# Optimization experiments

Hardware: AMD Instinct MI355X
Metric: run time of the kernel (lower is better)

The kernel has to match this reference:

```python
import jax, jax.numpy as jnp
import numpy as np

# Acoustic FDTD constants (seistorch-style geometry)
NSHOTS, NT = 4, 512
NZ, NX = 256, 256
NRECS = 128
DT = 1e-3   # s
DH = 10.0   # m grid spacing


def setup_inputs() -> dict:
    key = jax.random.key(0)
    k1, k2, k3, k4, k5, k6 = jax.random.split(key, 6)
    x = jax.random.normal(k1, (NSHOTS, NT), dtype=jnp.float32)  # source wavelets
    # velocity model in [1500, 4000] m/s (CFL: dt*vmax/dh = 0.4 < stability limit)
    vp = 1500.0 + 2500.0 * jax.random.uniform(k2, (NZ, NX), dtype=jnp.float32)
    src_z = jax.random.randint(k3, (NSHOTS,), 0, NZ)
    src_x = jax.random.randint(k4, (NSHOTS,), 0, NX)
    rec_z = jax.random.randint(k5, (NSHOTS, NRECS), 0, NZ)
    rec_x = jax.random.randint(k6, (NSHOTS, NRECS), 0, NX)
    return {"x": x, "vp": vp, "src_z": src_z, "src_x": src_x,
            "rec_z": rec_z, "rec_x": rec_x}


def _laplacian(p):
    # 5-point stencil, zero Dirichlet boundary. p: (B, NZ, NX)
    pp = jnp.pad(p, ((0, 0), (1, 1), (1, 1)))
    return (pp[:, 2:, 1:-1] + pp[:, :-2, 1:-1]
            + pp[:, 1:-1, 2:] + pp[:, 1:-1, :-2]
            - 4.0 * p) / (DH * DH)


def reference(x, vp, src_z, src_x, rec_z, rec_x):
    shots = jnp.arange(NSHOTS)
    c2dt2 = (vp * DT) ** 2  # (NZ, NX), broadcast over shots

    def step(carry, wav_t):
        p_prev, p = carry
        # 2nd-order acoustic update (the PDE "cell")
        p_next = 2.0 * p - p_prev + c2dt2 * _laplacian(p)
        # source scatter-inject (super_source)
        p_next = p_next.at[shots, src_z, src_x].add(wav_t * DT * DT)
        # receiver gather (super_probes): (NSHOTS, NRECS)
        rec = p_next[shots[:, None], rec_z, rec_x]
        return (p, p_next), rec

    p0 = jnp.zeros((NSHOTS, NZ, NX), dtype=x.dtype)
    _, recs = jax.lax.scan(step, (p0, p0), x.T)  # recs: (NT, NSHOTS, NRECS)
    # (shots, time, receivers, n_receiver_types=1)
    return jnp.transpose(recs, (1, 0, 2))[..., None]
```

## Files before the change

### kernel.cpp

```cpp
#include <hip/hip_runtime.h>

#define NSHOTS 4
#define NT     512
#define NZ     256
#define NX     256
#define NRECS  128

static constexpr float DTf    = 0.001f;
static constexpr float INVDH2 = 1.0f / (10.0f * 10.0f);

#define KSTEPS 16
#define TILE   32
#define RPT    8
#define NPAIRS 4
#define NWAVES 8
#define BLOCK  512
#define NWG    (NSHOTS * 64)
#define NPHASE (NT / KSTEPS)

typedef float v2f __attribute__((ext_vector_type(2)));
typedef unsigned long long ull;

__device__ __forceinline__ float nbr_left(float v) {
  return __int_as_float(__builtin_amdgcn_update_dpp(
      0, __float_as_int(v), 0x138 , 0xf, 0xf, true));
}
__device__ __forceinline__ float nbr_right(float v) {
  return __int_as_float(__builtin_amdgcn_update_dpp(
      0, __float_as_int(v), 0x130 , 0xf, 0xf, true));
}

__device__ __forceinline__ ull pload(const ull* p) {
  return __hip_atomic_load(p, __ATOMIC_RELAXED, __HIP_MEMORY_SCOPE_AGENT);
}
__device__ __forceinline__ void pstore(ull* p, ull v) {
  __hip_atomic_store(p, v, __ATOMIC_RELAXED, __HIP_MEMORY_SCOPE_AGENT);
}

__device__ __forceinline__ ull pack_w(float cur, float prev, unsigned tg) {
  const unsigned hi = (__float_as_uint(prev) & ~3u) | tg;
  return ((ull)hi << 32) | (ull)__float_as_uint(cur);
}
__device__ __forceinline__ float w_cur(ull w) {
  return __uint_as_float((unsigned)w);
}
__device__ __forceinline__ float w_prev(ull w) {
  return __uint_as_float(((unsigned)(w >> 32)) & ~3u);
}
__device__ __forceinline__ unsigned tag_of(int q) {
  return ((unsigned)(q >> 1) % 3u) + 1u;
}

__global__ __launch_bounds__(BLOCK, 4) void wave_pk(
    ull* __restrict__ gA, ull* __restrict__ gB,
    const float* __restrict__ vp, const float* __restrict__ xwav,
    const int* __restrict__ src_z, const int* __restrict__ src_x,
    const int* __restrict__ rec_z, const int* __restrict__ rec_x,
    float* __restrict__ out)
{
  const int bid  = blockIdx.x;
  const int s    = bid >> 6;
  const int tz   = (bid >> 3) & 7;
  const int tx   = bid & 7;
  const int tid  = threadIdx.x;
  const int w    = tid >> 6;
  const int lane = tid & 63;

  const int gz0 = tz * TILE - KSTEPS;
  const int gx0 = tx * TILE - KSTEPS;
  const int gx  = gx0 + lane;
  const int zb  = w * RPT;

  __shared__ float haloTop[2][NWAVES][64];
  __shared__ float haloBot[2][NWAVES][64];
  __shared__ float recTile[2][TILE][TILE + 1];
  __shared__ int   cntS;
  __shared__ int   lzA[NRECS], lxA[NRECS];
  __shared__ unsigned pkA[NRECS];

  if (tid == 0) cntS = 0;
  __syncthreads();
  if (tid < NRECS) {
    const int lz = rec_z[s * NRECS + tid] - tz * TILE;
    const int lx = rec_x[s * NRECS + tid] - tx * TILE;
    lzA[tid] = lz; lxA[tid] = lx;
    if ((unsigned)lz < (unsigned)TILE && (unsigned)lx < (unsigned)TILE) {
      const int k = atomicAdd(&cntS, 1);
      pkA[k] = (unsigned)tid | ((unsigned)lz << 8) | ((unsigned)lx << 16);
    }
  }
  __syncthreads();
  const int nRec = cntS;
  int myR = 0, myLz = 0, myLx = 0;
  if (tid < nRec) {
    const unsigned p = pkA[tid];
    myR = p & 255; myLz = (p >> 8) & 31; myLx = (p >> 16) & 31;
  }
  const bool wbRow = (w >= 2 && w < 6) && (lane >= KSTEPS && lane < KSTEPS + TILE);
  const int  ilz   = (w - 2) * RPT;
  const int  ilx   = lane - KSTEPS;
  unsigned recMask = 0;
  if (wbRow) {
    for (int r = 0; r < NRECS; ++r)
      if (lxA[r] == ilx && (unsigned)(lzA[r] - ilz) < (unsigned)RPT)
        recMask |= 1u << (lzA[r] - ilz);
  }

  const int slz = src_z[s] - gz0;
  const int slx = src_x[s] - gx0;
  const bool srcMine = (slx == lane) && ((unsigned)(slz - zb) < (unsigned)RPT);
  const int  srcI = slz - zb;
  v2f srcM2[NPAIRS];
  #pragma unroll
  for (int p = 0; p < NPAIRS; ++p) {
    srcM2[p].x = (srcMine && srcI == 2 * p)     ? 1.0f : 0.0f;
    srcM2[p].y = (srcMine && srcI == 2 * p + 1) ? 1.0f : 0.0f;
  }

  const bool xok = (unsigned)gx < (unsigned)NX;
  int   offRow[RPT];
  bool  okRow[RPT];
  v2f a2[NPAIRS], b2[NPAIRS], c22[NPAIRS], d22[NPAIRS];
  unsigned okMask = 0;
  #pragma unroll
  for (int p = 0; p < NPAIRS; ++p) {
    #pragma unroll
    for (int h = 0; h < 2; ++h) {
      const int i  = 2 * p + h;
      const int gz = gz0 + zb + i;
      const bool ok = xok && ((unsigned)gz < (unsigned)NZ);
      okRow[i]  = ok;
      if (ok) okMask |= 1u << i;
      offRow[i] = ok ? ((s * NZ + gz) * NX + gx) : 0;
      float v = ok ? vp[gz * NX + gx] : 0.0f;
      v *= DTf;
      const float c2 = v * v * INVDH2;
      if (h == 0) { c22[p].x = c2; d22[p].x = 2.0f - 4.0f * c2; }
      else        { c22[p].y = c2; d22[p].y = 2.0f - 4.0f * c2; }
    }
    a2[p] = (v2f)(0.0f); b2[p] = (v2f)(0.0f);
  }

  #pragma unroll 1
  for (int ph = 0; ph < NPHASE; ++ph) {
    const int t0 = ph * KSTEPS;

    float amp[KSTEPS];
    {
      const float4* xw4 = (const float4*)(xwav + s * NT + t0);
      #pragma unroll
      for (int q = 0; q < KSTEPS / 4; ++q) {
        const float4 v = xw4[q];
        amp[4 * q + 0] = (v.x * DTf) * DTf;
        amp[4 * q + 1] = (v.y * DTf) * DTf;
        amp[4 * q + 2] = (v.z * DTf) * DTf;
        amp[4 * q + 3] = (v.w * DTf) * DTf;
      }
    }

    if (ph > 0 && !wbRow) {
      const ull* gR = (ph & 1) ? gA : gB;
      const unsigned tg = tag_of(ph - 1);
      ull vw[RPT];
      unsigned need = okMask;
      while (need) {
        ull t[RPT];
        #pragma unroll
        for (int i = 0; i < RPT; ++i)
          if (need & (1u << i)) t[i] = pload(gR + offRow[i]);
        #pragma unroll
        for (int i = 0; i < RPT; ++i)
          if ((need & (1u << i)) && (((unsigned)(t[i] >> 32)) & 3u) == tg) {
            vw[i] = t[i];
            need &= ~(1u << i);
          }
        if (need) __builtin_amdgcn_s_sleep(1);
      }
      #pragma unroll
      for (int i = 0; i < RPT; ++i) {
        const float cv = okRow[i] ? w_cur(vw[i])  : 0.0f;
        const float pv = okRow[i] ? w_prev(vw[i]) : 0.0f;
        if (i & 1) { a2[i >> 1].y = cv; b2[i >> 1].y = pv; }
        else       { a2[i >> 1].x = cv; b2[i >> 1].x = pv; }
      }
    }

    float recv[KSTEPS];

    auto do_step = [&](v2f (&cur)[NPAIRS], v2f (&nxt)[NPAIRS], int tau) {
      const int pb = tau & 1;
      haloTop[pb][w][lane] = cur[0].x;
      haloBot[pb][w][lane] = cur[NPAIRS - 1].y;
      __syncthreads();
      if (tau > 0 && tid < nRec) recv[tau - 1] = recTile[1 - pb][myLz][myLx];
      const float up0 = (w > 0)          ? haloBot[pb][w - 1][lane] : 0.0f;
      const float dn7 = (w < NWAVES - 1) ? haloTop[pb][w + 1][lane] : 0.0f;
      const v2f av = { amp[tau], amp[tau] };
      #pragma unroll
      for (int p = 0; p < NPAIRS; ++p) {
        const float cx = cur[p].x, cy = cur[p].y;
        const float upx = (p == 0)          ? up0 : cur[p - 1].y;
        const float dny = (p == NPAIRS - 1) ? dn7 : cur[p + 1].x;
        v2f ud, lr;
        ud.x = upx + cy;
        ud.y = cx + dny;
        lr.x = nbr_left(cx) + nbr_right(cx);
        lr.y = nbr_left(cy) + nbr_right(cy);
        const v2f sum = ud + lr;
        v2f t = __builtin_elementwise_fma(c22[p], sum, -nxt[p]);
        t = __builtin_elementwise_fma(d22[p], cur[p], t);
        t = __builtin_elementwise_fma(srcM2[p], av, t);
        nxt[p] = t;
      }
      if (recMask) {
        #pragma unroll
        for (int i = 0; i < RPT; ++i)
          if (recMask & (1u << i))
            recTile[pb][ilz + i][ilx] = (i & 1) ? nxt[i >> 1].y : nxt[i >> 1].x;
      }
    };

    #pragma unroll
    for (int h = 0; h < KSTEPS / 2; ++h) {
      do_step(a2, b2, 2 * h);
      do_step(b2, a2, 2 * h + 1);
    }

    if (ph != NPHASE - 1) {
      ull* gW = (ph & 1) ? gB : gA;
      const unsigned tgw = tag_of(ph);
      if (wbRow) {
        #pragma unroll
        for (int p = 0; p < NPAIRS; ++p) {
          pstore(gW + offRow[2 * p],     pack_w(a2[p].x, b2[p].x, tgw));
          pstore(gW + offRow[2 * p + 1], pack_w(a2[p].y, b2[p].y, tgw));
        }
      }
    }
    __syncthreads();

    if (tid < nRec) {
      recv[KSTEPS - 1] = recTile[1][myLz][myLx];
      #pragma unroll
      for (int t = 0; t < KSTEPS; ++t)
        out[(s * NT + (t0 + t)) * NRECS + myR] = recv[t];
    }
  }
}

extern "C" void kernel_launch(void* const* d_in, const int* in_sizes, int n_in,
                              void* d_out, int out_size, void* d_ws, size_t ws_size,
                              hipStream_t stream) {
  const float* x     = (const float*)d_in[0];
  const float* vp    = (const float*)d_in[1];
  const int*   src_z = (const int*)d_in[2];
  const int*   src_x = (const int*)d_in[3];
  const int*   rec_z = (const int*)d_in[4];
  const int*   rec_x = (const int*)d_in[5];
  float* out = (float*)d_out;

  const size_t F = (size_t)NSHOTS * NZ * NX;
  ull* gA = (ull*)d_ws;
  ull* gB = gA + F;

  hipMemsetAsync(gA, 0, 2 * F * sizeof(ull), stream);

  wave_pk<<<dim3(NWG), dim3(BLOCK), 0, stream>>>(
      gA, gB, vp, x, src_z, src_x, rec_z, rec_x, out);
}
```

Before: 303.8 us.

## Widen per-wave slabs with two-row ghosts to sync once per two steps

Each wave now holds its 8-row slab plus two ghost rows on each side (12 rows in 6 pairs). Halos are exchanged through shared memory only every two time steps, which halves the number of block barriers. Receiver values are written straight to global memory from the owning lane each step, replacing the shared recTile staging and per-phase flush. The source amplitude is loaded and injected only in the wave that owns the source. In exchange there is redundant stencil work on the ghost rows, higher register pressure, and launch bounds lowered from 4 to 2 blocks per CU, which may reduce occupancy.

```diff
diff --git a/kernel.cpp b/kernel.cpp
--- a/kernel.cpp
+++ b/kernel.cpp
@@ -11,8 +11,8 @@
 
 #define KSTEPS 16
 #define TILE   32
-#define RPT    8
-#define NPAIRS 4
+#define SLAB   8
+#define WPAIR  6
 #define NWAVES 8
 #define BLOCK  512
 #define NWG    (NSHOTS * 64)
@@ -51,7 +51,7 @@
   return ((unsigned)(q >> 1) % 3u) + 1u;
 }
 
-__global__ __launch_bounds__(BLOCK, 4) void wave_pk(
+__global__ __launch_bounds__(BLOCK, 2) void wave_pk(
     ull* __restrict__ gA, ull* __restrict__ gB,
     const float* __restrict__ vp, const float* __restrict__ xwav,
     const int* __restrict__ src_z, const int* __restrict__ src_x,
@@ -69,69 +69,31 @@
   const int gz0 = tz * TILE - KSTEPS;
   const int gx0 = tx * TILE - KSTEPS;
   const int gx  = gx0 + lane;
-  const int zb  = w * RPT;
-
-  __shared__ float haloTop[2][NWAVES][64];
-  __shared__ float haloBot[2][NWAVES][64];
-  __shared__ float recTile[2][TILE][TILE + 1];
-  __shared__ int   cntS;
-  __shared__ int   lzA[NRECS], lxA[NRECS];
-  __shared__ unsigned pkA[NRECS];
-
-  if (tid == 0) cntS = 0;
-  __syncthreads();
-  if (tid < NRECS) {
-    const int lz = rec_z[s * NRECS + tid] - tz * TILE;
-    const int lx = rec_x[s * NRECS + tid] - tx * TILE;
-    lzA[tid] = lz; lxA[tid] = lx;
-    if ((unsigned)lz < (unsigned)TILE && (unsigned)lx < (unsigned)TILE) {
-      const int k = atomicAdd(&cntS, 1);
-      pkA[k] = (unsigned)tid | ((unsigned)lz << 8) | ((unsigned)lx << 16);
-    }
-  }
-  __syncthreads();
-  const int nRec = cntS;
-  int myR = 0, myLz = 0, myLx = 0;
-  if (tid < nRec) {
-    const unsigned p = pkA[tid];
-    myR = p & 255; myLz = (p >> 8) & 31; myLx = (p >> 16) & 31;
-  }
-  const bool wbRow = (w >= 2 && w < 6) && (lane >= KSTEPS && lane < KSTEPS + TILE);
-  const int  ilz   = (w - 2) * RPT;
-  const int  ilx   = lane - KSTEPS;
-  unsigned recMask = 0;
-  if (wbRow) {
-    for (int r = 0; r < NRECS; ++r)
-      if (lxA[r] == ilx && (unsigned)(lzA[r] - ilz) < (unsigned)RPT)
-        recMask |= 1u << (lzA[r] - ilz);
-  }
-
-  const int slz = src_z[s] - gz0;
-  const int slx = src_x[s] - gx0;
-  const bool srcMine = (slx == lane) && ((unsigned)(slz - zb) < (unsigned)RPT);
-  const int  srcI = slz - zb;
-  v2f srcM2[NPAIRS];
-  #pragma unroll
-  for (int p = 0; p < NPAIRS; ++p) {
-    srcM2[p].x = (srcMine && srcI == 2 * p)     ? 1.0f : 0.0f;
-    srcM2[p].y = (srcMine && srcI == 2 * p + 1) ? 1.0f : 0.0f;
-  }
-
+  const int zb  = w * SLAB;
   const bool xok = (unsigned)gx < (unsigned)NX;
-  int   offRow[RPT];
-  bool  okRow[RPT];
-  v2f a2[NPAIRS], b2[NPAIRS], c22[NPAIRS], d22[NPAIRS];
+
+  __shared__ float xchC[2][NWAVES][4][64];
+  __shared__ float xchP[NWAVES][2][64];
+  __shared__ int   lzS[NRECS], lxS[NRECS];
+
+  int offRow[SLAB];
   unsigned okMask = 0;
   #pragma unroll
-  for (int p = 0; p < NPAIRS; ++p) {
+  for (int k = 0; k < SLAB; ++k) {
+    const int gz = gz0 + zb + k;
+    const bool ok = xok && (unsigned)gz < (unsigned)NZ;
+    offRow[k] = ok ? ((s * NZ + gz) * NX + gx) : 0;
+    if (ok) okMask |= 1u << k;
+  }
+
+  v2f c22[WPAIR], d22[WPAIR], a2[WPAIR], b2[WPAIR];
+  #pragma unroll
+  for (int p = 0; p < WPAIR; ++p) {
     #pragma unroll
     for (int h = 0; h < 2; ++h) {
-      const int i  = 2 * p + h;
-      const int gz = gz0 + zb + i;
-      const bool ok = xok && ((unsigned)gz < (unsigned)NZ);
-      okRow[i]  = ok;
-      if (ok) okMask |= 1u << i;
-      offRow[i] = ok ? ((s * NZ + gz) * NX + gx) : 0;
+      const int e  = zb - 2 + 2 * p + h;
+      const int gz = gz0 + e;
+      const bool ok = ((unsigned)e < 64u) && xok && ((unsigned)gz < (unsigned)NZ);
       float v = ok ? vp[gz * NX + gx] : 0.0f;
       v *= DTf;
       const float c2 = v * v * INVDH2;
@@ -141,12 +103,126 @@
     a2[p] = (v2f)(0.0f); b2[p] = (v2f)(0.0f);
   }
 
+  const bool wbT = (w >= 2 && w < 6) && (lane >= KSTEPS && lane < KSTEPS + TILE);
+
+  if (tid < NRECS) {
+    lzS[tid] = rec_z[s * NRECS + tid] - tz * TILE;
+    lxS[tid] = rec_x[s * NRECS + tid] - tx * TILE;
+  }
+  __syncthreads();
+  unsigned e0 = 0, e1 = 0, rB0 = 0, rB1 = 0, rB2 = 0, rB3 = 0;
+  if (wbT) {
+    int cnt = 0;
+    #pragma unroll 1
+    for (int r = 0; r < NRECS; ++r) {
+      const int er = lzS[r], ex = lxS[r];
+      if ((unsigned)er < (unsigned)TILE && (unsigned)ex < (unsigned)TILE) {
+        const int extz = er + KSTEPS;
+        if ((extz >> 3) == w && ex + KSTEPS == lane) {
+          const int wr = extz - zb + 2;
+          const unsigned e = 0x8000u | ((unsigned)wr << 8) | (unsigned)r;
+          if (cnt == 0) e0 = e;
+          else if (cnt == 1) e1 = e;
+          else {
+            if (r < 32)      rB0 |= 1u << r;
+            else if (r < 64) rB1 |= 1u << (r - 32);
+            else if (r < 96) rB2 |= 1u << (r - 64);
+            else             rB3 |= 1u << (r - 96);
+          }
+          ++cnt;
+        }
+      }
+    }
+  }
+  const bool hasOvf = (rB0 | rB1 | rB2 | rB3) != 0;
+
+  const int slz = src_z[s] - gz0;
+  const int slx = src_x[s] - gx0;
+  const int srcRow = slz - (zb - 2);
+  const bool hasSrc = ((unsigned)slz < 64u) && ((unsigned)slx < 64u) &&
+                      ((unsigned)srcRow < 12u);
+  const bool srcLane = (slx == lane);
+
+  float amp[KSTEPS];
+
+  auto selSlab = [](const v2f (&n)[WPAIR], int wr) -> float {
+    const int q = (wr >> 1) - 1;
+    const v2f pA = (q & 1) ? n[2] : n[1];
+    const v2f pB = (q & 1) ? n[4] : n[3];
+    const v2f pp = (q & 2) ? pB : pA;
+    return (wr & 1) ? pp.y : pp.x;
+  };
+
+  auto do_step = [&](v2f (&cur)[WPAIR], v2f (&nxt)[WPAIR], int tau, int t0) {
+    #pragma unroll
+    for (int p = 0; p < WPAIR; ++p) {
+      const float cx = cur[p].x, cy = cur[p].y;
+      const float upx = (p == 0)         ? 0.0f : cur[p - 1].y;
+      const float dny = (p == WPAIR - 1) ? 0.0f : cur[p + 1].x;
+      v2f ud, lr;
+      ud.x = upx + cy;
+      ud.y = cx + dny;
+      lr.x = nbr_left(cx) + nbr_right(cx);
+      lr.y = nbr_left(cy) + nbr_right(cy);
+      const v2f sum = ud + lr;
+      v2f t = __builtin_elementwise_fma(c22[p], sum, -nxt[p]);
+      t = __builtin_elementwise_fma(d22[p], cur[p], t);
+      nxt[p] = t;
+    }
+    if (hasSrc) {
+      const float av = amp[tau];
+      #pragma unroll
+      for (int p = 0; p < WPAIR; ++p) {
+        if (srcLane && srcRow == 2 * p)     nxt[p].x += av;
+        if (srcLane && srcRow == 2 * p + 1) nxt[p].y += av;
+      }
+    }
+    const int t = t0 + tau;
+    if (e0 & 0x8000u)
+      out[(s * NT + t) * NRECS + (e0 & 127u)] = selSlab(nxt, (e0 >> 8) & 15);
+    if (e1 & 0x8000u)
+      out[(s * NT + t) * NRECS + (e1 & 127u)] = selSlab(nxt, (e1 >> 8) & 15);
+    if (hasOvf) {
+      #pragma unroll
+      for (int wd = 0; wd < 4; ++wd) {
+        unsigned m = (wd == 0) ? rB0 : (wd == 1) ? rB1 : (wd == 2) ? rB2 : rB3;
+        while (m) {
+          const int b = __builtin_ctz(m); m &= m - 1;
+          const int r = wd * 32 + b;
+          const int wr = lzS[r] + KSTEPS - zb + 2;
+          out[(s * NT + t) * NRECS + r] = selSlab(nxt, wr);
+        }
+      }
+    }
+  };
+
+  auto exchange = [&](int buf, bool withPrev) {
+    xchC[buf][w][0][lane] = a2[1].x;
+    xchC[buf][w][1][lane] = a2[1].y;
+    xchC[buf][w][2][lane] = a2[4].x;
+    xchC[buf][w][3][lane] = a2[4].y;
+    if (withPrev) {
+      xchP[w][0][lane] = b2[1].x;
+      xchP[w][1][lane] = b2[4].y;
+    }
+    __syncthreads();
+    if (w > 0) {
+      a2[0].x = xchC[buf][w - 1][2][lane];
+      a2[0].y = xchC[buf][w - 1][3][lane];
+      if (withPrev) b2[0].y = xchP[w - 1][1][lane];
+    }
+    if (w < NWAVES - 1) {
+      a2[5].x = xchC[buf][w + 1][0][lane];
+      a2[5].y = xchC[buf][w + 1][1][lane];
+      if (withPrev) b2[5].x = xchP[w + 1][0][lane];
+    }
+  };
+
   #pragma unroll 1
   for (int ph = 0; ph < NPHASE; ++ph) {
     const int t0 = ph * KSTEPS;
 
-    float amp[KSTEPS];
-    {
+    if (hasSrc) {
       const float4* xw4 = (const float4*)(xwav + s * NT + t0);
       #pragma unroll
       for (int q = 0; q < KSTEPS / 4; ++q) {
@@ -158,18 +234,18 @@
       }
     }
 
-    if (ph > 0 && !wbRow) {
+    if (ph > 0 && !wbT) {
       const ull* gR = (ph & 1) ? gA : gB;
       const unsigned tg = tag_of(ph - 1);
-      ull vw[RPT];
+      ull vw[SLAB];
       unsigned need = okMask;
       while (need) {
-        ull t[RPT];
+        ull t[SLAB];
         #pragma unroll
-        for (int i = 0; i < RPT; ++i)
+        for (int i = 0; i < SLAB; ++i)
           if (need & (1u << i)) t[i] = pload(gR + offRow[i]);
         #pragma unroll
-        for (int i = 0; i < RPT; ++i)
+        for (int i = 0; i < SLAB; ++i)
           if ((need & (1u << i)) && (((unsigned)(t[i] >> 32)) & 3u) == tg) {
             vw[i] = t[i];
             need &= ~(1u << i);
@@ -177,73 +253,33 @@
         if (need) __builtin_amdgcn_s_sleep(1);
       }
       #pragma unroll
-      for (int i = 0; i < RPT; ++i) {
-        const float cv = okRow[i] ? w_cur(vw[i])  : 0.0f;
-        const float pv = okRow[i] ? w_prev(vw[i]) : 0.0f;
-        if (i & 1) { a2[i >> 1].y = cv; b2[i >> 1].y = pv; }
-        else       { a2[i >> 1].x = cv; b2[i >> 1].x = pv; }
-      }
-    }
-
-    float recv[KSTEPS];
-
-    auto do_step = [&](v2f (&cur)[NPAIRS], v2f (&nxt)[NPAIRS], int tau) {
-      const int pb = tau & 1;
-      haloTop[pb][w][lane] = cur[0].x;
-      haloBot[pb][w][lane] = cur[NPAIRS - 1].y;
-      __syncthreads();
-      if (tau > 0 && tid < nRec) recv[tau - 1] = recTile[1 - pb][myLz][myLx];
-      const float up0 = (w > 0)          ? haloBot[pb][w - 1][lane] : 0.0f;
-      const float dn7 = (w < NWAVES - 1) ? haloTop[pb][w + 1][lane] : 0.0f;
-      const v2f av = { amp[tau], amp[tau] };
-      #pragma unroll
-      for (int p = 0; p < NPAIRS; ++p) {
-        const float cx = cur[p].x, cy = cur[p].y;
-        const float upx = (p == 0)          ? up0 : cur[p - 1].y;
-        const float dny = (p == NPAIRS - 1) ? dn7 : cur[p + 1].x;
-        v2f ud, lr;
-        ud.x = upx + cy;
-        ud.y = cx + dny;
-        lr.x = nbr_left(cx) + nbr_right(cx);
-        lr.y = nbr_left(cy) + nbr_right(cy);
-        const v2f sum = ud + lr;
-        v2f t = __builtin_elementwise_fma(c22[p], sum, -nxt[p]);
-        t = __builtin_elementwise_fma(d22[p], cur[p], t);
-        t = __builtin_elementwise_fma(srcM2[p], av, t);
-        nxt[p] = t;
-      }
-      if (recMask) {
-        #pragma unroll
-        for (int i = 0; i < RPT; ++i)
-          if (recMask & (1u << i))
-            recTile[pb][ilz + i][ilx] = (i & 1) ? nxt[i >> 1].y : nxt[i >> 1].x;
-      }
-    };
+      for (int k = 0; k < SLAB; ++k) {
+        const bool ok = (okMask >> k) & 1;
+        const float cv = ok ? w_cur(vw[k])  : 0.0f;
+        const float pv = ok ? w_prev(vw[k]) : 0.0f;
+        const int p = 1 + (k >> 1);
+        if (k & 1) { a2[p].y = cv; b2[p].y = pv; }
+        else       { a2[p].x = cv; b2[p].x = pv; }
+      }
+    }
 
     #pragma unroll
-    for (int h = 0; h < KSTEPS / 2; ++h) {
-      do_step(a2, b2, 2 * h);
-      do_step(b2, a2, 2 * h + 1);
-    }
-
-    if (ph != NPHASE - 1) {
+    for (int blk = 0; blk < KSTEPS / 2; ++blk) {
+      exchange(blk & 1, blk == 0);
+      do_step(a2, b2, 2 * blk,     t0);
+      do_step(b2, a2, 2 * blk + 1, t0);
+    }
+
+    if (ph != NPHASE - 1 && wbT) {
       ull* gW = (ph & 1) ? gB : gA;
       const unsigned tgw = tag_of(ph);
-      if (wbRow) {
-        #pragma unroll
-        for (int p = 0; p < NPAIRS; ++p) {
-          pstore(gW + offRow[2 * p],     pack_w(a2[p].x, b2[p].x, tgw));
-          pstore(gW + offRow[2 * p + 1], pack_w(a2[p].y, b2[p].y, tgw));
-        }
-      }
-    }
-    __syncthreads();
-
-    if (tid < nRec) {
-      recv[KSTEPS - 1] = recTile[1][myLz][myLx];
-      #pragma unroll
-      for (int t = 0; t < KSTEPS; ++t)
-        out[(s * NT + (t0 + t)) * NRECS + myR] = recv[t];
+      #pragma unroll
+      for (int k = 0; k < SLAB; ++k) {
+        const int p = 1 + (k >> 1);
+        const float cv = (k & 1) ? a2[p].y : a2[p].x;
+        const float pv = (k & 1) ? b2[p].y : b2[p].x;
+        pstore(gW + offRow[k], pack_w(cv, pv, tgw));
+      }
     }
   }
 }
```

Result: slower. 358.9 us (+18.2%).

## Replace per-step block barriers with neighbor-wave LDS flag synchronization

Applied to the files above, without the earlier changes.

Each time step previously ended in a workgroup-wide __syncthreads. Now each wave waits only on its two vertical neighbor waves through per-wave LDS flags with acquire/release semantics. Receiver samples are written straight to global memory by the owning lane instead of staging through a shared tile. Source injection and wavelet loads are restricted to the wave that contains the source. Launch bounds drop from 4 to 2 blocks per SM, and the spin-waiting can stall or cost issue slots if waves drift apart.

```diff
diff --git a/kernel.cpp b/kernel.cpp
--- a/kernel.cpp
+++ b/kernel.cpp
@@ -17,6 +17,7 @@
 #define BLOCK  512
 #define NWG    (NSHOTS * 64)
 #define NPHASE (NT / KSTEPS)
+#define FSTR   32
 
 typedef float v2f __attribute__((ext_vector_type(2)));
 typedef unsigned long long ull;
@@ -51,7 +52,14 @@
   return ((unsigned)(q >> 1) % 3u) + 1u;
 }
 
-__global__ __launch_bounds__(BLOCK, 4) void wave_pk(
+__device__ __forceinline__ int lflag(const int* p) {
+  return __hip_atomic_load(p, __ATOMIC_ACQUIRE, __HIP_MEMORY_SCOPE_WORKGROUP);
+}
+__device__ __forceinline__ void sflag(int* p, int v) {
+  __hip_atomic_store(p, v, __ATOMIC_RELEASE, __HIP_MEMORY_SCOPE_WORKGROUP);
+}
+
+__global__ __launch_bounds__(BLOCK, 2) void wave_pk(
     ull* __restrict__ gA, ull* __restrict__ gB,
     const float* __restrict__ vp, const float* __restrict__ xwav,
     const int* __restrict__ src_z, const int* __restrict__ src_x,
@@ -71,55 +79,25 @@
   const int gx  = gx0 + lane;
   const int zb  = w * RPT;
 
-  __shared__ float haloTop[2][NWAVES][64];
-  __shared__ float haloBot[2][NWAVES][64];
-  __shared__ float recTile[2][TILE][TILE + 1];
-  __shared__ int   cntS;
-  __shared__ int   lzA[NRECS], lxA[NRECS];
-  __shared__ unsigned pkA[NRECS];
-
-  if (tid == 0) cntS = 0;
-  __syncthreads();
+  __shared__ float hT[2][NWAVES][64];
+  __shared__ float hB[2][NWAVES][64];
+  __shared__ int   wfl[NWAVES * FSTR];
+  __shared__ int   lzS[NRECS], lxS[NRECS];
+
   if (tid < NRECS) {
-    const int lz = rec_z[s * NRECS + tid] - tz * TILE;
-    const int lx = rec_x[s * NRECS + tid] - tx * TILE;
-    lzA[tid] = lz; lxA[tid] = lx;
-    if ((unsigned)lz < (unsigned)TILE && (unsigned)lx < (unsigned)TILE) {
-      const int k = atomicAdd(&cntS, 1);
-      pkA[k] = (unsigned)tid | ((unsigned)lz << 8) | ((unsigned)lx << 16);
-    }
-  }
-  __syncthreads();
-  const int nRec = cntS;
-  int myR = 0, myLz = 0, myLx = 0;
-  if (tid < nRec) {
-    const unsigned p = pkA[tid];
-    myR = p & 255; myLz = (p >> 8) & 31; myLx = (p >> 16) & 31;
-  }
-  const bool wbRow = (w >= 2 && w < 6) && (lane >= KSTEPS && lane < KSTEPS + TILE);
-  const int  ilz   = (w - 2) * RPT;
-  const int  ilx   = lane - KSTEPS;
-  unsigned recMask = 0;
-  if (wbRow) {
-    for (int r = 0; r < NRECS; ++r)
-      if (lxA[r] == ilx && (unsigned)(lzA[r] - ilz) < (unsigned)RPT)
-        recMask |= 1u << (lzA[r] - ilz);
-  }
-
-  const int slz = src_z[s] - gz0;
-  const int slx = src_x[s] - gx0;
-  const bool srcMine = (slx == lane) && ((unsigned)(slz - zb) < (unsigned)RPT);
-  const int  srcI = slz - zb;
-  v2f srcM2[NPAIRS];
-  #pragma unroll
-  for (int p = 0; p < NPAIRS; ++p) {
-    srcM2[p].x = (srcMine && srcI == 2 * p)     ? 1.0f : 0.0f;
-    srcM2[p].y = (srcMine && srcI == 2 * p + 1) ? 1.0f : 0.0f;
-  }
+    lzS[tid] = rec_z[s * NRECS + tid] - tz * TILE;
+    lxS[tid] = rec_x[s * NRECS + tid] - tx * TILE;
+  }
+  hT[0][w][lane] = 0.0f; hB[0][w][lane] = 0.0f;
+  hT[1][w][lane] = 0.0f; hB[1][w][lane] = 0.0f;
+  if (lane == 0)
+    __hip_atomic_store(&wfl[w * FSTR], 0, __ATOMIC_RELAXED,
+                       __HIP_MEMORY_SCOPE_WORKGROUP);
+
+  const bool wbT = (w >= 2 && w < 6) && (lane >= KSTEPS && lane < KSTEPS + TILE);
 
   const bool xok = (unsigned)gx < (unsigned)NX;
   int   offRow[RPT];
-  bool  okRow[RPT];
   v2f a2[NPAIRS], b2[NPAIRS], c22[NPAIRS], d22[NPAIRS];
   unsigned okMask = 0;
   #pragma unroll
@@ -129,7 +107,6 @@
       const int i  = 2 * p + h;
       const int gz = gz0 + zb + i;
       const bool ok = xok && ((unsigned)gz < (unsigned)NZ);
-      okRow[i]  = ok;
       if (ok) okMask |= 1u << i;
       offRow[i] = ok ? ((s * NZ + gz) * NX + gx) : 0;
       float v = ok ? vp[gz * NX + gx] : 0.0f;
@@ -141,12 +118,114 @@
     a2[p] = (v2f)(0.0f); b2[p] = (v2f)(0.0f);
   }
 
+  const int slz = src_z[s] - gz0;
+  const int slx = src_x[s] - gx0;
+  const bool hasSrcW = ((unsigned)slx < 64u) &&
+                       ((unsigned)(slz - zb) < (unsigned)RPT);
+  const bool srcMine = hasSrcW && (slx == lane);
+  const int  srcI = slz - zb;
+  v2f srcM2[NPAIRS];
+  #pragma unroll
+  for (int p = 0; p < NPAIRS; ++p) {
+    srcM2[p].x = (srcMine && srcI == 2 * p)     ? 1.0f : 0.0f;
+    srcM2[p].y = (srcMine && srcI == 2 * p + 1) ? 1.0f : 0.0f;
+  }
+
+  __syncthreads();
+
+  unsigned e0 = 0, e1 = 0, rB0 = 0, rB1 = 0, rB2 = 0, rB3 = 0;
+  if (wbT) {
+    int cnt = 0;
+    #pragma unroll 1
+    for (int r = 0; r < NRECS; ++r) {
+      const int er = lzS[r], ex = lxS[r];
+      if ((unsigned)er < (unsigned)TILE && (unsigned)ex < (unsigned)TILE) {
+        const int extz = er + KSTEPS;
+        if ((extz >> 3) == w && ex + KSTEPS == lane) {
+          const unsigned e = 0x8000u | ((unsigned)(extz & 7) << 8) | (unsigned)r;
+          if (cnt == 0) e0 = e;
+          else if (cnt == 1) e1 = e;
+          else {
+            if (r < 32)      rB0 |= 1u << r;
+            else if (r < 64) rB1 |= 1u << (r - 32);
+            else if (r < 96) rB2 |= 1u << (r - 64);
+            else             rB3 |= 1u << (r - 96);
+          }
+          ++cnt;
+        }
+      }
+    }
+  }
+  const bool hasOvf = (rB0 | rB1 | rB2 | rB3) != 0;
+
+  float amp[KSTEPS];
+
+  auto selRow = [](const v2f (&n)[NPAIRS], int row) -> float {
+    const v2f pA = (row & 2) ? n[1] : n[0];
+    const v2f pB = (row & 2) ? n[3] : n[2];
+    const v2f pp = (row & 4) ? pB : pA;
+    return (row & 1) ? pp.y : pp.x;
+  };
+
+  auto do_step = [&](v2f (&cur)[NPAIRS], v2f (&nxt)[NPAIRS], int tau, int t0) {
+    const int tg = t0 + tau + 1;
+    if (w > 0)
+      while (lflag(&wfl[(w - 1) * FSTR]) < tg - 1) {}
+    if (w < NWAVES - 1)
+      while (lflag(&wfl[(w + 1) * FSTR]) < tg - 1) {}
+    const int rs = (tg - 1) & 1;
+    const float up0 = (w > 0)          ? hB[rs][w - 1][lane] : 0.0f;
+    const float dn7 = (w < NWAVES - 1) ? hT[rs][w + 1][lane] : 0.0f;
+    #pragma unroll
+    for (int p = 0; p < NPAIRS; ++p) {
+      const float cx = cur[p].x, cy = cur[p].y;
+      const float upx = (p == 0)          ? up0 : cur[p - 1].y;
+      const float dny = (p == NPAIRS - 1) ? dn7 : cur[p + 1].x;
+      v2f ud, lr;
+      ud.x = upx + cy;
+      ud.y = cx + dny;
+      lr.x = nbr_left(cx) + nbr_right(cx);
+      lr.y = nbr_left(cy) + nbr_right(cy);
+      const v2f sum = ud + lr;
+      v2f t = __builtin_elementwise_fma(c22[p], sum, -nxt[p]);
+      t = __builtin_elementwise_fma(d22[p], cur[p], t);
+      nxt[p] = t;
+    }
+    if (hasSrcW) {
+      const v2f av = { amp[tau], amp[tau] };
+      #pragma unroll
+      for (int p = 0; p < NPAIRS; ++p)
+        nxt[p] = __builtin_elementwise_fma(srcM2[p], av, nxt[p]);
+    }
+    if (tau != KSTEPS - 1) {
+      const int ws2 = tg & 1;
+      hT[ws2][w][lane] = nxt[0].x;
+      hB[ws2][w][lane] = nxt[NPAIRS - 1].y;
+      if (lane == 0) sflag(&wfl[w * FSTR], tg);
+    }
+    const int t = t0 + tau;
+    if (e0 & 0x8000u)
+      out[(s * NT + t) * NRECS + (e0 & 127u)] = selRow(nxt, (e0 >> 8) & 7);
+    if (e1 & 0x8000u)
+      out[(s * NT + t) * NRECS + (e1 & 127u)] = selRow(nxt, (e1 >> 8) & 7);
+    if (hasOvf) {
+      #pragma unroll
+      for (int wd = 0; wd < 4; ++wd) {
+        unsigned m = (wd == 0) ? rB0 : (wd == 1) ? rB1 : (wd == 2) ? rB2 : rB3;
+        while (m) {
+          const int b = __builtin_ctz(m); m &= m - 1;
+          const int r = wd * 32 + b;
+          out[(s * NT + t) * NRECS + r] = selRow(nxt, (lzS[r] + KSTEPS) & 7);
+        }
+      }
+    }
+  };
+
   #pragma unroll 1
   for (int ph = 0; ph < NPHASE; ++ph) {
     const int t0 = ph * KSTEPS;
 
-    float amp[KSTEPS];
-    {
+    if (hasSrcW) {
       const float4* xw4 = (const float4*)(xwav + s * NT + t0);
       #pragma unroll
       for (int q = 0; q < KSTEPS / 4; ++q) {
@@ -158,92 +237,53 @@
       }
     }
 
-    if (ph > 0 && !wbRow) {
-      const ull* gR = (ph & 1) ? gA : gB;
-      const unsigned tg = tag_of(ph - 1);
-      ull vw[RPT];
-      unsigned need = okMask;
-      while (need) {
-        ull t[RPT];
+    if (ph > 0) {
+      if (!wbT) {
+        const ull* gR = (ph & 1) ? gA : gB;
+        const unsigned tg = tag_of(ph - 1);
+        ull vw[RPT];
+        unsigned need = okMask;
+        while (need) {
+          ull t[RPT];
+          #pragma unroll
+          for (int i = 0; i < RPT; ++i)
+            if (need & (1u << i)) t[i] = pload(gR + offRow[i]);
+          #pragma unroll
+          for (int i = 0; i < RPT; ++i)
+            if ((need & (1u << i)) && (((unsigned)(t[i] >> 32)) & 3u) == tg) {
+              vw[i] = t[i];
+              need &= ~(1u << i);
+            }
+          if (need) __builtin_amdgcn_s_sleep(1);
+        }
         #pragma unroll
-        for (int i = 0; i < RPT; ++i)
-          if (need & (1u << i)) t[i] = pload(gR + offRow[i]);
-        #pragma unroll
-        for (int i = 0; i < RPT; ++i)
-          if ((need & (1u << i)) && (((unsigned)(t[i] >> 32)) & 3u) == tg) {
-            vw[i] = t[i];
-            need &= ~(1u << i);
-          }
-        if (need) __builtin_amdgcn_s_sleep(1);
-      }
-      #pragma unroll
-      for (int i = 0; i < RPT; ++i) {
-        const float cv = okRow[i] ? w_cur(vw[i])  : 0.0f;
-        const float pv = okRow[i] ? w_prev(vw[i]) : 0.0f;
-        if (i & 1) { a2[i >> 1].y = cv; b2[i >> 1].y = pv; }
-        else       { a2[i >> 1].x = cv; b2[i >> 1].x = pv; }
-      }
-    }
-
-    float recv[KSTEPS];
-
-    auto do_step = [&](v2f (&cur)[NPAIRS], v2f (&nxt)[NPAIRS], int tau) {
-      const int pb = tau & 1;
-      haloTop[pb][w][lane] = cur[0].x;
-      haloBot[pb][w][lane] = cur[NPAIRS - 1].y;
-      __syncthreads();
-      if (tau > 0 && tid < nRec) recv[tau - 1] = recTile[1 - pb][myLz][myLx];
-      const float up0 = (w > 0)          ? haloBot[pb][w - 1][lane] : 0.0f;
-      const float dn7 = (w < NWAVES - 1) ? haloTop[pb][w + 1][lane] : 0.0f;
-      const v2f av = { amp[tau], amp[tau] };
+        for (int i = 0; i < RPT; ++i) {
+          const bool ok = (okMask >> i) & 1;
+          const float cv = ok ? w_cur(vw[i])  : 0.0f;
+          const float pv = ok ? w_prev(vw[i]) : 0.0f;
+          if (i & 1) { a2[i >> 1].y = cv; b2[i >> 1].y = pv; }
+          else       { a2[i >> 1].x = cv; b2[i >> 1].x = pv; }
+        }
+      }
+      hT[0][w][lane] = a2[0].x;
+      hB[0][w][lane] = a2[NPAIRS - 1].y;
+      if (lane == 0) sflag(&wfl[w * FSTR], t0);
+    }
+
+    #pragma unroll
+    for (int h = 0; h < KSTEPS / 2; ++h) {
+      do_step(a2, b2, 2 * h,     t0);
+      do_step(b2, a2, 2 * h + 1, t0);
+    }
+
+    if (ph != NPHASE - 1 && wbT) {
+      ull* gW = (ph & 1) ? gB : gA;
+      const unsigned tgw = tag_of(ph);
       #pragma unroll
       for (int p = 0; p < NPAIRS; ++p) {
-        const float cx = cur[p].x, cy = cur[p].y;
-        const float upx = (p == 0)          ? up0 : cur[p - 1].y;
-        const float dny = (p == NPAIRS - 1) ? dn7 : cur[p + 1].x;
-        v2f ud, lr;
-        ud.x = upx + cy;
-        ud.y = cx + dny;
-        lr.x = nbr_left(cx) + nbr_right(cx);
-        lr.y = nbr_left(cy) + nbr_right(cy);
-        const v2f sum = ud + lr;
-        v2f t = __builtin_elementwise_fma(c22[p], sum, -nxt[p]);
-        t = __builtin_elementwise_fma(d22[p], cur[p], t);
-        t = __builtin_elementwise_fma(srcM2[p], av, t);
-        nxt[p] = t;
-      }
-      if (recMask) {
-        #pragma unroll
-        for (int i = 0; i < RPT; ++i)
-          if (recMask & (1u << i))
-            recTile[pb][ilz + i][ilx] = (i & 1) ? nxt[i >> 1].y : nxt[i >> 1].x;
-      }
-    };
-
-    #pragma unroll
-    for (int h = 0; h < KSTEPS / 2; ++h) {
-      do_step(a2, b2, 2 * h);
-      do_step(b2, a2, 2 * h + 1);
-    }
-
-    if (ph != NPHASE - 1) {
-      ull* gW = (ph & 1) ? gB : gA;
-      const unsigned tgw = tag_of(ph);
-      if (wbRow) {
-        #pragma unroll
-        for (int p = 0; p < NPAIRS; ++p) {
-          pstore(gW + offRow[2 * p],     pack_w(a2[p].x, b2[p].x, tgw));
-          pstore(gW + offRow[2 * p + 1], pack_w(a2[p].y, b2[p].y, tgw));
-        }
-      }
-    }
-    __syncthreads();
-
-    if (tid < nRec) {
-      recv[KSTEPS - 1] = recTile[1][myLz][myLx];
-      #pragma unroll
-      for (int t = 0; t < KSTEPS; ++t)
-        out[(s * NT + (t0 + t)) * NRECS + myR] = recv[t];
+        pstore(gW + offRow[2 * p],     pack_w(a2[p].x, b2[p].x, tgw));
+        pstore(gW + offRow[2 * p + 1], pack_w(a2[p].y, b2[p].y, tgw));
+      }
     }
   }
 }
```

Measured after the change: 316.5 us. 4.2% more time.

## Interleave two shots per workgroup with flag-based wave sync and smaller tiles

Applied to the files above, without the earlier changes.

Each workgroup now handles two shots on 16x32 tiles with 8-step temporal blocking, and interleaves the two shots' time steps offset by half a phase. The goal is to hide global halo exchange latency behind the other shot's compute. Per-step __syncthreads is replaced with per-wave LDS flags for neighbour-only sync. Receiver values are written directly from registers instead of through a shared tile, and the halo reads are prefetched. The cost is more registers and harder-to-verify flag protocols, and the occupancy bound drops to 2 blocks per SIMD.

```diff
diff --git a/kernel.cpp b/kernel.cpp
--- a/kernel.cpp
+++ b/kernel.cpp
@@ -9,14 +9,17 @@
 static constexpr float DTf    = 0.001f;
 static constexpr float INVDH2 = 1.0f / (10.0f * 10.0f);
 
-#define KSTEPS 16
-#define TILE   32
-#define RPT    8
-#define NPAIRS 4
+#define KS     8
+#define TILEZ  16
+#define TILEX  32
+#define RPW    4
+#define NPR    2
 #define NWAVES 8
 #define BLOCK  512
-#define NWG    (NSHOTS * 64)
-#define NPHASE (NT / KSTEPS)
+#define NWG    256
+#define NPH    (NT / KS)
+#define FSTR   32
+#define SHOT2  (2 * NZ * NX)
 
 typedef float v2f __attribute__((ext_vector_type(2)));
 typedef unsigned long long ull;
@@ -41,9 +44,7 @@
   const unsigned hi = (__float_as_uint(prev) & ~3u) | tg;
   return ((ull)hi << 32) | (ull)__float_as_uint(cur);
 }
-__device__ __forceinline__ float w_cur(ull w) {
-  return __uint_as_float((unsigned)w);
-}
+__device__ __forceinline__ float w_cur(ull w)  { return __uint_as_float((unsigned)w); }
 __device__ __forceinline__ float w_prev(ull w) {
   return __uint_as_float(((unsigned)(w >> 32)) & ~3u);
 }
@@ -51,7 +52,15 @@
   return ((unsigned)(q >> 1) % 3u) + 1u;
 }
 
-__global__ __launch_bounds__(BLOCK, 4) void wave_pk(
+__device__ __forceinline__ int frel(const int* p) {
+  return __hip_atomic_load(p, __ATOMIC_RELAXED, __HIP_MEMORY_SCOPE_WORKGROUP);
+}
+__device__ __forceinline__ void fput(int* p, int v) {
+  __builtin_amdgcn_fence(__ATOMIC_RELEASE, "workgroup");
+  __hip_atomic_store(p, v, __ATOMIC_RELAXED, __HIP_MEMORY_SCOPE_WORKGROUP);
+}
+
+__global__ __launch_bounds__(BLOCK, 2) void wave_pk(
     ull* __restrict__ gA, ull* __restrict__ gB,
     const float* __restrict__ vp, const float* __restrict__ xwav,
     const int* __restrict__ src_z, const int* __restrict__ src_x,
@@ -59,191 +68,303 @@
     float* __restrict__ out)
 {
   const int bid  = blockIdx.x;
-  const int s    = bid >> 6;
-  const int tz   = (bid >> 3) & 7;
+  const int sA   = bid >> 7;
+  const int sB   = sA + 2;
+  const int tz   = (bid >> 3) & 15;
   const int tx   = bid & 7;
   const int tid  = threadIdx.x;
   const int w    = tid >> 6;
   const int lane = tid & 63;
 
-  const int gz0 = tz * TILE - KSTEPS;
-  const int gx0 = tx * TILE - KSTEPS;
+  const int gz0 = tz * TILEZ - KS;
+  const int gx0 = tx * TILEX - KS;
   const int gx  = gx0 + lane;
-  const int zb  = w * RPT;
-
-  __shared__ float haloTop[2][NWAVES][64];
-  __shared__ float haloBot[2][NWAVES][64];
-  __shared__ float recTile[2][TILE][TILE + 1];
-  __shared__ int   cntS;
-  __shared__ int   lzA[NRECS], lxA[NRECS];
-  __shared__ unsigned pkA[NRECS];
-
-  if (tid == 0) cntS = 0;
-  __syncthreads();
+  const int zb  = w * RPW;
+  const bool xok = (unsigned)gx < (unsigned)NX;
+
+  __shared__ float hTA[2][NWAVES][64], hBA[2][NWAVES][64];
+  __shared__ float hTB[2][NWAVES][64], hBB[2][NWAVES][64];
+  __shared__ int   flA[NWAVES * FSTR], flB[NWAVES * FSTR];
+  __shared__ int   lzT[2][NRECS], lxT[2][NRECS];
+
+  hTA[0][w][lane] = 0.0f; hBA[0][w][lane] = 0.0f;
+  hTA[1][w][lane] = 0.0f; hBA[1][w][lane] = 0.0f;
+  hTB[0][w][lane] = 0.0f; hBB[0][w][lane] = 0.0f;
+  hTB[1][w][lane] = 0.0f; hBB[1][w][lane] = 0.0f;
+  if (lane == 0) {
+    __hip_atomic_store(&flA[w * FSTR], 0, __ATOMIC_RELAXED, __HIP_MEMORY_SCOPE_WORKGROUP);
+    __hip_atomic_store(&flB[w * FSTR], 0, __ATOMIC_RELAXED, __HIP_MEMORY_SCOPE_WORKGROUP);
+  }
   if (tid < NRECS) {
-    const int lz = rec_z[s * NRECS + tid] - tz * TILE;
-    const int lx = rec_x[s * NRECS + tid] - tx * TILE;
-    lzA[tid] = lz; lxA[tid] = lx;
-    if ((unsigned)lz < (unsigned)TILE && (unsigned)lx < (unsigned)TILE) {
-      const int k = atomicAdd(&cntS, 1);
-      pkA[k] = (unsigned)tid | ((unsigned)lz << 8) | ((unsigned)lx << 16);
-    }
-  }
-  __syncthreads();
-  const int nRec = cntS;
-  int myR = 0, myLz = 0, myLx = 0;
-  if (tid < nRec) {
-    const unsigned p = pkA[tid];
-    myR = p & 255; myLz = (p >> 8) & 31; myLx = (p >> 16) & 31;
-  }
-  const bool wbRow = (w >= 2 && w < 6) && (lane >= KSTEPS && lane < KSTEPS + TILE);
-  const int  ilz   = (w - 2) * RPT;
-  const int  ilx   = lane - KSTEPS;
-  unsigned recMask = 0;
-  if (wbRow) {
-    for (int r = 0; r < NRECS; ++r)
-      if (lxA[r] == ilx && (unsigned)(lzA[r] - ilz) < (unsigned)RPT)
-        recMask |= 1u << (lzA[r] - ilz);
-  }
-
-  const int slz = src_z[s] - gz0;
-  const int slx = src_x[s] - gx0;
-  const bool srcMine = (slx == lane) && ((unsigned)(slz - zb) < (unsigned)RPT);
-  const int  srcI = slz - zb;
-  v2f srcM2[NPAIRS];
+    lzT[0][tid] = rec_z[sA * NRECS + tid] - tz * TILEZ;
+    lxT[0][tid] = rec_x[sA * NRECS + tid] - tx * TILEX;
+    lzT[1][tid] = rec_z[sB * NRECS + tid] - tz * TILEZ;
+    lxT[1][tid] = rec_x[sB * NRECS + tid] - tx * TILEX;
+  }
+
+  int offRow[RPW]; unsigned okM = 0;
+  v2f c22[NPR], d22[NPR], aA[NPR], bA[NPR], aB[NPR], bB[NPR];
   #pragma unroll
-  for (int p = 0; p < NPAIRS; ++p) {
-    srcM2[p].x = (srcMine && srcI == 2 * p)     ? 1.0f : 0.0f;
-    srcM2[p].y = (srcMine && srcI == 2 * p + 1) ? 1.0f : 0.0f;
-  }
-
-  const bool xok = (unsigned)gx < (unsigned)NX;
-  int   offRow[RPT];
-  bool  okRow[RPT];
-  v2f a2[NPAIRS], b2[NPAIRS], c22[NPAIRS], d22[NPAIRS];
-  unsigned okMask = 0;
-  #pragma unroll
-  for (int p = 0; p < NPAIRS; ++p) {
+  for (int p = 0; p < NPR; ++p) {
     #pragma unroll
     for (int h = 0; h < 2; ++h) {
-      const int i  = 2 * p + h;
-      const int gz = gz0 + zb + i;
+      const int i = 2 * p + h, gz = gz0 + zb + i;
       const bool ok = xok && ((unsigned)gz < (unsigned)NZ);
-      okRow[i]  = ok;
-      if (ok) okMask |= 1u << i;
-      offRow[i] = ok ? ((s * NZ + gz) * NX + gx) : 0;
+      if (ok) okM |= 1u << i;
+      offRow[i] = ok ? ((sA * NZ + gz) * NX + gx) : 0;
       float v = ok ? vp[gz * NX + gx] : 0.0f;
       v *= DTf;
       const float c2 = v * v * INVDH2;
       if (h == 0) { c22[p].x = c2; d22[p].x = 2.0f - 4.0f * c2; }
       else        { c22[p].y = c2; d22[p].y = 2.0f - 4.0f * c2; }
     }
-    a2[p] = (v2f)(0.0f); b2[p] = (v2f)(0.0f);
-  }
-
-  #pragma unroll 1
-  for (int ph = 0; ph < NPHASE; ++ph) {
-    const int t0 = ph * KSTEPS;
-
-    float amp[KSTEPS];
-    {
-      const float4* xw4 = (const float4*)(xwav + s * NT + t0);
+    aA[p] = (v2f)(0.0f); bA[p] = (v2f)(0.0f);
+    aB[p] = (v2f)(0.0f); bB[p] = (v2f)(0.0f);
+  }
+  const bool wbT = (w >= 2 && w < 6) &&
+                   ((unsigned)(lane - KS) < (unsigned)TILEX);
+  const unsigned rlM = wbT ? 0u : okM;
+
+  v2f smA[NPR], smB[NPR]; bool hsA, hsB;
+  {
+    const int slz = src_z[sA] - gz0, slx = src_x[sA] - gx0;
+    const int si = slz - zb;
+    hsA = ((unsigned)slx < 64u) && ((unsigned)si < (unsigned)RPW);
+    const bool mine = hsA && (slx == lane);
+    smA[0].x = (mine && si == 0) ? 1.f : 0.f; smA[0].y = (mine && si == 1) ? 1.f : 0.f;
+    smA[1].x = (mine && si == 2) ? 1.f : 0.f; smA[1].y = (mine && si == 3) ? 1.f : 0.f;
+  }
+  {
+    const int slz = src_z[sB] - gz0, slx = src_x[sB] - gx0;
+    const int si = slz - zb;
+    hsB = ((unsigned)slx < 64u) && ((unsigned)si < (unsigned)RPW);
+    const bool mine = hsB && (slx == lane);
+    smB[0].x = (mine && si == 0) ? 1.f : 0.f; smB[0].y = (mine && si == 1) ? 1.f : 0.f;
+    smB[1].x = (mine && si == 2) ? 1.f : 0.f; smB[1].y = (mine && si == 3) ? 1.f : 0.f;
+  }
+
+  __syncthreads();
+
+  unsigned e0A = 0, e1A = 0, ovA[4] = {0, 0, 0, 0};
+  unsigned e0B = 0, e1B = 0, ovB[4] = {0, 0, 0, 0};
+  if (wbT) {
+    int cA = 0, cB = 0;
+    #pragma unroll 1
+    for (int r = 0; r < NRECS; ++r) {
+      {
+        const int er = lzT[0][r], ex = lxT[0][r];
+        if ((unsigned)er < (unsigned)TILEZ && (unsigned)ex < (unsigned)TILEX) {
+          const int extz = er + KS;
+          if ((extz >> 2) == w && ex + KS == lane) {
+            const unsigned e = 0x8000u | ((unsigned)(extz & 3) << 8) | (unsigned)r;
+            if (cA == 0) e0A = e; else if (cA == 1) e1A = e;
+            else ovA[r >> 5] |= 1u << (r & 31);
+            ++cA;
+          }
+        }
+      }
+      {
+        const int er = lzT[1][r], ex = lxT[1][r];
+        if ((unsigned)er < (unsigned)TILEZ && (unsigned)ex < (unsigned)TILEX) {
+          const int extz = er + KS;
+          if ((extz >> 2) == w && ex + KS == lane) {
+            const unsigned e = 0x8000u | ((unsigned)(extz & 3) << 8) | (unsigned)r;
+            if (cB == 0) e0B = e; else if (cB == 1) e1B = e;
+            else ovB[r >> 5] |= 1u << (r & 31);
+            ++cB;
+          }
+        }
+      }
+    }
+  }
+  const bool hOvA = (ovA[0] | ovA[1] | ovA[2] | ovA[3]) != 0;
+  const bool hOvB = (ovB[0] | ovB[1] | ovB[2] | ovB[3]) != 0;
+
+  auto selRow = [](const v2f (&n)[NPR], int ri) -> float {
+    const v2f pp = (ri & 2) ? n[1] : n[0];
+    return (ri & 1) ? pp.y : pp.x;
+  };
+
+  auto stepT = [&](v2f (&cur)[NPR], v2f (&nxt)[NPR], auto& hT, auto& hB,
+                   int* fl, const v2f (&sm)[NPR], bool hs, float av,
+                   bool pub, int u) {
+    for (;;) {
+      int fm = 0x7fffffff, fp = 0x7fffffff;
+      if (w > 0)          fm = frel(&fl[(w - 1) * FSTR]);
+      if (w < NWAVES - 1) fp = frel(&fl[(w + 1) * FSTR]);
+      if (fm >= u && fp >= u) break;
+    }
+    __builtin_amdgcn_fence(__ATOMIC_ACQUIRE, "workgroup");
+    const int sl = u & 1;
+    const float up0 = (w > 0)          ? hB[sl][w - 1][lane] : 0.0f;
+    const float dn  = (w < NWAVES - 1) ? hT[sl][w + 1][lane] : 0.0f;
+    #pragma unroll
+    for (int p = 0; p < NPR; ++p) {
+      const float cx = cur[p].x, cy = cur[p].y;
+      const float upx = (p == 0)       ? up0 : cur[p - 1].y;
+      const float dny = (p == NPR - 1) ? dn  : cur[p + 1].x;
+      v2f ud, lr;
+      ud.x = upx + cy;
+      ud.y = cx + dny;
+      lr.x = nbr_left(cx) + nbr_right(cx);
+      lr.y = nbr_left(cy) + nbr_right(cy);
+      const v2f sum = ud + lr;
+      v2f t = __builtin_elementwise_fma(c22[p], sum, -nxt[p]);
+      t = __builtin_elementwise_fma(d22[p], cur[p], t);
+      nxt[p] = t;
+    }
+    if (hs) {
+      const v2f av2 = { av, av };
+      nxt[0] = __builtin_elementwise_fma(sm[0], av2, nxt[0]);
+      nxt[1] = __builtin_elementwise_fma(sm[1], av2, nxt[1]);
+    }
+    if (pub) {
+      hT[(u + 1) & 1][w][lane] = nxt[0].x;
+      hB[(u + 1) & 1][w][lane] = nxt[1].y;
+      if (lane == 0) fput(&fl[w * FSTR], u + 1);
+    }
+  };
+
+  auto recst = [&](const v2f (&n)[NPR], int t, int s, unsigned e0, unsigned e1,
+                   bool hOv, const unsigned (&ov)[4], const int* lz) {
+    if (e0 & 0x8000u) out[(s * NT + t) * NRECS + (e0 & 127u)] = selRow(n, (e0 >> 8) & 3);
+    if (e1 & 0x8000u) out[(s * NT + t) * NRECS + (e1 & 127u)] = selRow(n, (e1 >> 8) & 3);
+    if (hOv) {
       #pragma unroll
-      for (int q = 0; q < KSTEPS / 4; ++q) {
-        const float4 v = xw4[q];
-        amp[4 * q + 0] = (v.x * DTf) * DTf;
-        amp[4 * q + 1] = (v.y * DTf) * DTf;
-        amp[4 * q + 2] = (v.z * DTf) * DTf;
-        amp[4 * q + 3] = (v.w * DTf) * DTf;
-      }
-    }
-
-    if (ph > 0 && !wbRow) {
-      const ull* gR = (ph & 1) ? gA : gB;
-      const unsigned tg = tag_of(ph - 1);
-      ull vw[RPT];
-      unsigned need = okMask;
-      while (need) {
-        ull t[RPT];
-        #pragma unroll
-        for (int i = 0; i < RPT; ++i)
-          if (need & (1u << i)) t[i] = pload(gR + offRow[i]);
-        #pragma unroll
-        for (int i = 0; i < RPT; ++i)
-          if ((need & (1u << i)) && (((unsigned)(t[i] >> 32)) & 3u) == tg) {
-            vw[i] = t[i];
-            need &= ~(1u << i);
-          }
-        if (need) __builtin_amdgcn_s_sleep(1);
-      }
+      for (int wd = 0; wd < 4; ++wd) {
+        unsigned m = ov[wd];
+        while (m) {
+          const int b = __builtin_ctz(m); m &= m - 1;
+          const int r = wd * 32 + b;
+          out[(s * NT + t) * NRECS + r] = selRow(n, (lz[r] + KS) & 3);
+        }
+      }
+    }
+  };
+
+  auto checkRe = [&](ull (&pr)[RPW], const ull* base, unsigned tg,
+                     v2f (&a2)[NPR], v2f (&b2)[NPR]) {
+    unsigned need = rlM;
+    #pragma unroll
+    for (int i = 0; i < RPW; ++i)
+      if ((need >> i) & 1)
+        if ((((unsigned)(pr[i] >> 32)) & 3u) == tg) need &= ~(1u << i);
+    while (need) {
+      ull t[RPW];
       #pragma unroll
-      for (int i = 0; i < RPT; ++i) {
-        const float cv = okRow[i] ? w_cur(vw[i])  : 0.0f;
-        const float pv = okRow[i] ? w_prev(vw[i]) : 0.0f;
+      for (int i = 0; i < RPW; ++i)
+        if ((need >> i) & 1) t[i] = pload(base + offRow[i]);
+      #pragma unroll
+      for (int i = 0; i < RPW; ++i)
+        if (((need >> i) & 1) && ((((unsigned)(t[i] >> 32)) & 3u) == tg)) {
+          pr[i] = t[i]; need &= ~(1u << i);
+        }
+      if (need) __builtin_amdgcn_s_sleep(1);
+    }
+    #pragma unroll
+    for (int i = 0; i < RPW; ++i)
+      if ((rlM >> i) & 1) {
+        const float cv = w_cur(pr[i]), pv = w_prev(pr[i]);
         if (i & 1) { a2[i >> 1].y = cv; b2[i >> 1].y = pv; }
         else       { a2[i >> 1].x = cv; b2[i >> 1].x = pv; }
       }
-    }
-
-    float recv[KSTEPS];
-
-    auto do_step = [&](v2f (&cur)[NPAIRS], v2f (&nxt)[NPAIRS], int tau) {
-      const int pb = tau & 1;
-      haloTop[pb][w][lane] = cur[0].x;
-      haloBot[pb][w][lane] = cur[NPAIRS - 1].y;
-      __syncthreads();
-      if (tau > 0 && tid < nRec) recv[tau - 1] = recTile[1 - pb][myLz][myLx];
-      const float up0 = (w > 0)          ? haloBot[pb][w - 1][lane] : 0.0f;
-      const float dn7 = (w < NWAVES - 1) ? haloTop[pb][w + 1][lane] : 0.0f;
-      const v2f av = { amp[tau], amp[tau] };
+  };
+  auto prefIssue = [&](ull (&pr)[RPW], const ull* base) {
+    #pragma unroll
+    for (int i = 0; i < RPW; ++i)
+      if ((rlM >> i) & 1) pr[i] = pload(base + offRow[i]);
+  };
+  auto wbStore = [&](ull* base, unsigned tg, const v2f (&a2)[NPR],
+                     const v2f (&b2)[NPR]) {
+    if (wbT) {
       #pragma unroll
-      for (int p = 0; p < NPAIRS; ++p) {
-        const float cx = cur[p].x, cy = cur[p].y;
-        const float upx = (p == 0)          ? up0 : cur[p - 1].y;
-        const float dny = (p == NPAIRS - 1) ? dn7 : cur[p + 1].x;
-        v2f ud, lr;
-        ud.x = upx + cy;
-        ud.y = cx + dny;
-        lr.x = nbr_left(cx) + nbr_right(cx);
-        lr.y = nbr_left(cy) + nbr_right(cy);
-        const v2f sum = ud + lr;
-        v2f t = __builtin_elementwise_fma(c22[p], sum, -nxt[p]);
-        t = __builtin_elementwise_fma(d22[p], cur[p], t);
-        t = __builtin_elementwise_fma(srcM2[p], av, t);
-        nxt[p] = t;
-      }
-      if (recMask) {
-        #pragma unroll
-        for (int i = 0; i < RPT; ++i)
-          if (recMask & (1u << i))
-            recTile[pb][ilz + i][ilx] = (i & 1) ? nxt[i >> 1].y : nxt[i >> 1].x;
-      }
-    };
-
-    #pragma unroll
-    for (int h = 0; h < KSTEPS / 2; ++h) {
-      do_step(a2, b2, 2 * h);
-      do_step(b2, a2, 2 * h + 1);
-    }
-
-    if (ph != NPHASE - 1) {
-      ull* gW = (ph & 1) ? gB : gA;
-      const unsigned tgw = tag_of(ph);
-      if (wbRow) {
-        #pragma unroll
-        for (int p = 0; p < NPAIRS; ++p) {
-          pstore(gW + offRow[2 * p],     pack_w(a2[p].x, b2[p].x, tgw));
-          pstore(gW + offRow[2 * p + 1], pack_w(a2[p].y, b2[p].y, tgw));
-        }
-      }
-    }
-    __syncthreads();
-
-    if (tid < nRec) {
-      recv[KSTEPS - 1] = recTile[1][myLz][myLx];
-      #pragma unroll
-      for (int t = 0; t < KSTEPS; ++t)
-        out[(s * NT + (t0 + t)) * NRECS + myR] = recv[t];
+      for (int i = 0; i < RPW; ++i) {
+        const float cv = (i & 1) ? a2[i >> 1].y : a2[i >> 1].x;
+        const float pv = (i & 1) ? b2[i >> 1].y : b2[i >> 1].x;
+        pstore(base + offRow[i], pack_w(cv, pv, tg));
+      }
+    }
+  };
+
+  float ampA[KS], ampB[KS];
+  ull prA[RPW], prB[RPW];
+
+  #pragma unroll 1
+  for (int ph = 0; ph <= NPH; ++ph) {
+    if (ph < NPH) {
+      if (ph > 0) {
+        const ull* rb = ((ph - 1) & 1) ? gB : gA;
+        checkRe(prA, rb, tag_of(ph - 1), aA, bA);
+      }
+      hTA[0][w][lane] = aA[0].x;
+      hBA[0][w][lane] = aA[1].y;
+      if (lane == 0) fput(&flA[w * FSTR], 8 * ph);
+      if (hsA) {
+        const float4 v = *(const float4*)(xwav + sA * NT + 8 * ph);
+        const float4 u4 = *(const float4*)(xwav + sA * NT + 8 * ph + 4);
+        ampA[0] = v.x * DTf * DTf;  ampA[1] = v.y * DTf * DTf;
+        ampA[2] = v.z * DTf * DTf;  ampA[3] = v.w * DTf * DTf;
+        ampA[4] = u4.x * DTf * DTf; ampA[5] = u4.y * DTf * DTf;
+        ampA[6] = u4.z * DTf * DTf; ampA[7] = u4.w * DTf * DTf;
+      }
+    }
+
+    #pragma unroll
+    for (int tau = 0; tau < 8; ++tau) {
+      const int u = 8 * ph + tau;
+
+      if (ph < NPH) {
+        if ((tau & 1) == 0) {
+          stepT(aA, bA, hTA, hBA, flA, smA, hsA, ampA[tau], tau != 7, u);
+          recst(bA, u, sA, e0A, e1A, hOvA, ovA, lzT[0]);
+        } else {
+          stepT(bA, aA, hTA, hBA, flA, smA, hsA, ampA[tau], tau != 7, u);
+          recst(aA, u, sA, e0A, e1A, hOvA, ovA, lzT[0]);
+        }
+      }
+
+      if (tau == 4 && ph < NPH) {
+        if (ph > 0) {
+          const ull* rb = (((ph - 1) & 1) ? gB : gA) + SHOT2;
+          checkRe(prB, rb, tag_of(ph - 1), aB, bB);
+        }
+        hTB[0][w][lane] = aB[0].x;
+        hBB[0][w][lane] = aB[1].y;
+        if (lane == 0) fput(&flB[w * FSTR], 8 * ph);
+        if (hsB) {
+          const float4 v = *(const float4*)(xwav + sB * NT + 8 * ph);
+          const float4 u4 = *(const float4*)(xwav + sB * NT + 8 * ph + 4);
+          ampB[0] = v.x * DTf * DTf;  ampB[1] = v.y * DTf * DTf;
+          ampB[2] = v.z * DTf * DTf;  ampB[3] = v.w * DTf * DTf;
+          ampB[4] = u4.x * DTf * DTf; ampB[5] = u4.y * DTf * DTf;
+          ampB[6] = u4.z * DTf * DTf; ampB[7] = u4.w * DTf * DTf;
+        }
+      }
+
+      {
+        const int g = u - 4;
+        if (g >= 0 && g < NT) {
+          const float av = ampB[(tau + 4) & 7];
+          if ((tau & 1) == 0) {
+            stepT(aB, bB, hTB, hBB, flB, smB, hsB, av, (g & 7) != 7, g);
+            recst(bB, g, sB, e0B, e1B, hOvB, ovB, lzT[1]);
+          } else {
+            stepT(bB, aB, hTB, hBB, flB, smB, hsB, av, (g & 7) != 7, g);
+            recst(aB, g, sB, e0B, e1B, hOvB, ovB, lzT[1]);
+          }
+        }
+      }
+
+      if (tau == 3 && ph >= 1 && ph < NPH) {
+        ull* basew = (((ph - 1) & 1) ? gB : gA) + SHOT2;
+        wbStore(basew, tag_of(ph - 1), aB, bB);
+        prefIssue(prB, basew);
+      }
+      if (tau == 7 && ph < NPH - 1) {
+        ull* basew = (ph & 1) ? gB : gA;
+        wbStore(basew, tag_of(ph), aA, bA);
+        prefIssue(prA, basew);
+      }
     }
   }
 }
```

After: 927.6 us. 205% more time.
